# Kernel optimization log

Measured on AMD Instinct MI355X. Metric: run time of the kernel, lower is better.

The kernel has to match this reference:

```python
import jax, jax.numpy as jnp
import numpy as np

B, C, H, W = 2, 256, 64, 64
NUM_HEADS = 8


def setup_inputs() -> dict:
    key = jax.random.key(0)
    k1, k2, k3 = jax.random.split(key, 3)
    x = jax.random.normal(k1, (B, C, H, W), dtype=jnp.float32)
    # 1x1 convs, bias=False -> plain [out_ch, in_ch] matrices
    w_qkv = jax.random.normal(k2, (3 * C, C), dtype=jnp.float32) * (1.0 / np.sqrt(C))
    w_proj = jax.random.normal(k3, (C, C), dtype=jnp.float32) * (1.0 / np.sqrt(C))
    return {"x": x, "w_qkv": w_qkv, "w_proj": w_proj}


def reference(x, w_qkv, w_proj):
    b, c, h, w = x.shape
    hd = NUM_HEADS
    d = c // hd  # head dim
    n = h * w    # number of tokens

    # 1x1 conv == channel matmul: [3C, C] x [B, C, H, W] -> [B, 3C, H, W]
    qkv = jnp.einsum('oc,bchw->bohw', w_qkv, x)
    q, k, v = jnp.split(qkv, 3, axis=1)

    def reshape(t):
        return t.reshape(b, hd, d, n)  # [B, h, d, N]

    q, k, v = map(reshape, (q, k, v))

    # scores[b,h,i,j] = sum_d q[b,h,d,i] * k[b,h,d,j] / sqrt(d)
    scores = jnp.einsum('bhdi,bhdj->bhij', q, k) / jnp.sqrt(jnp.asarray(d, x.dtype))
    attn = jax.nn.softmax(scores, axis=-1)

    # out[b,h,d,i] = sum_j attn[b,h,i,j] * v[b,h,d,j]
    out = jnp.einsum('bhij,bhdj->bhdi', attn, v)
    out = out.reshape(b, c, h, w)

    return jnp.einsum('oc,bchw->bohw', w_proj, out) + x
```

## Files before the change

### kernel.cpp

```cpp
#include <hip/hip_runtime.h>
#include <hip/hip_bf16.h>

#define NB  2
#define CC  256
#define NHD 8
#define HD  32
#define NT  4096

typedef __bf16 bf16x8 __attribute__((ext_vector_type(8)));
typedef bf16x8 bf16x8_ma __attribute__((may_alias));
typedef __bf16 bf16x4 __attribute__((ext_vector_type(4)));
typedef bf16x4 bf16x4_ma __attribute__((may_alias));
typedef float  f32x4  __attribute__((ext_vector_type(4)));
typedef f32x4  f32x4_ma __attribute__((may_alias));
typedef float  f32x16 __attribute__((ext_vector_type(16)));
typedef unsigned int u32x4 __attribute__((ext_vector_type(4)));
typedef unsigned short u16x8 __attribute__((ext_vector_type(8)));

static __device__ __forceinline__ f32x4 zero4() {
    f32x4 z = {0.f, 0.f, 0.f, 0.f}; return z;
}
static __device__ __forceinline__ f32x16 zero16() {
    f32x16 z = {0.f,0.f,0.f,0.f,0.f,0.f,0.f,0.f,
                0.f,0.f,0.f,0.f,0.f,0.f,0.f,0.f};
    return z;
}

#define QSCALE 0.25505392421795654f

#define CVT_PK(dst, lo, hi_) \
    asm("v_cvt_pk_bf16_f32 %0, %1, %2" : "=v"(dst) : "v"(lo), "v"(hi_))
#define PLSWAP(x, y) \
    asm("v_permlane32_swap_b32 %0, %1" : "+v"(x), "+v"(y))


__global__ __launch_bounds__(256) void convw_k(const float* __restrict__ s1,
                                               __bf16* __restrict__ d1, int n1,
                                               const float* __restrict__ s2,
                                               __bf16* __restrict__ d2, int n2) {
    const int i = blockIdx.x * 256 + threadIdx.x;
    if (i < n1) d1[i] = (__bf16)s1[i];
    else if (i - n1 < n2) d2[i - n1] = (__bf16)s2[i - n1];
}

__global__ __launch_bounds__(256) void qkv_k(const __bf16* __restrict__ wqkv,
                                             const float* __restrict__ x,
                                             __bf16* __restrict__ qt,
                                             __bf16* __restrict__ kt,
                                             __bf16* __restrict__ vv) {
    __shared__ __align__(16) __bf16 T[64][264];

    const int tid  = threadIdx.x;
    const int lane = tid & 63, wv = tid >> 6;
    const int g = lane >> 4, c16 = lane & 15;
    const int b    = blockIdx.z;
    const int o0   = blockIdx.y * 64 + wv * 16;
    const int tok0 = blockIdx.x * 64;

    {
        const int tok4 = (tid & 15) * 4;
        const int crow = tid >> 4;
#pragma unroll
        for (int i = 0; i < 16; ++i) {
            const int c = i * 16 + crow;
            f32x4 v = *(const f32x4_ma*)&x[((size_t)(b * CC + c)) * NT + tok0 + tok4];
#pragma unroll
            for (int j = 0; j < 4; ++j)
                T[tok4 + j][c] = (__bf16)v[j];
        }
    }

    const __bf16* arow = wqkv + (size_t)(o0 + c16) * CC + g * 8;
    bf16x8 a[8];
#pragma unroll
    for (int kc = 0; kc < 8; ++kc) a[kc] = *(const bf16x8_ma*)(arow + kc * 32);

    __syncthreads();

    f32x4 acc[4];
#pragma unroll
    for (int i = 0; i < 4; ++i) acc[i] = zero4();

#pragma unroll
    for (int kc = 0; kc < 8; ++kc) {
#pragma unroll
        for (int js = 0; js < 4; ++js) {
            bf16x8 bb = *(const bf16x8_ma*)&T[js * 16 + c16][kc * 32 + g * 8];
            acc[js] = __builtin_amdgcn_mfma_f32_16x16x32_bf16(a[kc], bb, acc[js], 0, 0, 0);
        }
    }

    const int reg = o0 >> 8;
    const int oo0 = (o0 & 255) + g * 4;
    const int h   = oo0 >> 5;
    const int dd0 = oo0 & 31;
    const size_t bh = (size_t)(b * NHD + h);

#pragma unroll
    for (int js = 0; js < 4; ++js) {
        const int tok = tok0 + js * 16 + c16;
        if (reg == 0) {
            bf16x4 pk;
#pragma unroll
            for (int r = 0; r < 4; ++r) pk[r] = (__bf16)(acc[js][r] * QSCALE);
            *(bf16x4_ma*)(qt + (bh * NT + tok) * HD + dd0) = pk;
        } else if (reg == 1) {
            bf16x4 pk;
#pragma unroll
            for (int r = 0; r < 4; ++r) pk[r] = (__bf16)acc[js][r];
            *(bf16x4_ma*)(kt + (bh * NT + tok) * HD + dd0) = pk;
        } else {
#pragma unroll
            for (int r = 0; r < 4; ++r)
                vv[(bh * HD + dd0 + r) * NT + tok] = (__bf16)acc[js][r];
        }
    }
}

__global__ __launch_bounds__(256, 4) void attn_k(const __bf16* __restrict__ qt,
                                                 const __bf16* __restrict__ kt,
                                                 const __bf16* __restrict__ vv,
                                                 __bf16* __restrict__ ao,
                                                 float* __restrict__ PO,
                                                 float* __restrict__ PL) {
    __shared__ __align__(16) __bf16 KF[2][4][2][512];
    __shared__ __align__(16) __bf16 VF[2][4][2][512];

    const int tid  = threadIdx.x;
    const int lane = tid & 63, wv = tid >> 6;
    const int c32 = lane & 31, hi = lane >> 5;
    const int bh = blockIdx.y;
    const int b = bh >> 3, h = bh & 7;
    const int seg = blockIdx.z, nseg = gridDim.z;
    const int i0q = blockIdx.x * 128 + wv * 32;

    const __bf16* qbase = qt + ((size_t)bh * NT + i0q) * HD;
    const __bf16* kbase = kt + (size_t)bh * NT * HD;
    const __bf16* vbase = vv + (size_t)bh * HD * NT;

    bf16x8 aq0 = *(const bf16x8_ma*)(qbase + (size_t)c32 * HD + hi * 8);
    bf16x8 aq1 = *(const bf16x8_ma*)(qbase + (size_t)c32 * HD + 16 + hi * 8);

    u16x8 ones_u = {0x3F80,0x3F80,0x3F80,0x3F80,0x3F80,0x3F80,0x3F80,0x3F80};
    const bf16x8 ones = __builtin_bit_cast(bf16x8, ones_u);

    f32x16 oacc = zero16();
    f32x16 lacc = zero16();

#define STAGE(bf, jb) do {                                                              \
    const __bf16* gk = kbase + (size_t)((jb) + wv * 32 + c32) * HD + hi * 8;            \
    __builtin_amdgcn_global_load_lds(                                                   \
        (const __attribute__((address_space(1))) void*)gk,                              \
        (__attribute__((address_space(3))) void*)&KF[bf][wv][0][0],                     \
        16, 0, 0);                                                                      \
    __builtin_amdgcn_global_load_lds(                                                   \
        (const __attribute__((address_space(1))) void*)(gk + 16),                       \
        (__attribute__((address_space(3))) void*)&KF[bf][wv][1][0],                     \
        16, 0, 0);                                                                      \
    const __bf16* gv = vbase + (size_t)c32 * NT + (jb) + wv * 32 + hi * 8;              \
    __builtin_amdgcn_global_load_lds(                                                   \
        (const __attribute__((address_space(1))) void*)gv,                              \
        (__attribute__((address_space(3))) void*)&VF[bf][wv][0][0],                     \
        16, 0, 0);                                                                      \
    __builtin_amdgcn_global_load_lds(                                                   \
        (const __attribute__((address_space(1))) void*)(gv + 16),                       \
        (__attribute__((address_space(3))) void*)&VF[bf][wv][1][0],                     \
        16, 0, 0);                                                                      \
} while (0)

#define SUBTILE(bf, js) do {                                                            \
    bf16x8 fk0 = *(const bf16x8_ma*)&KF[bf][js][0][lane * 8];                           \
    bf16x8 fk1 = *(const bf16x8_ma*)&KF[bf][js][1][lane * 8];                           \
    bf16x8 fv0 = *(const bf16x8_ma*)&VF[bf][js][0][lane * 8];                           \
    bf16x8 fv1 = *(const bf16x8_ma*)&VF[bf][js][1][lane * 8];                           \
    f32x16 s = __builtin_amdgcn_mfma_f32_32x32x16_bf16(fk0, aq0, zero16(), 0, 0, 0);    \
    s = __builtin_amdgcn_mfma_f32_32x32x16_bf16(fk1, aq1, s, 0, 0, 0);                  \
    float p[16];                                                                        \
    _Pragma("unroll")                                                                   \
    for (int r = 0; r < 16; ++r) p[r] = __builtin_amdgcn_exp2f(s[r]);                   \
    unsigned pk[8];                                                                     \
    _Pragma("unroll")                                                                   \
    for (int i = 0; i < 8; ++i) CVT_PK(pk[i], p[2 * i], p[2 * i + 1]);                  \
    PLSWAP(pk[0], pk[2]);                                                               \
    PLSWAP(pk[1], pk[3]);                                                               \
    PLSWAP(pk[4], pk[6]);                                                               \
    PLSWAP(pk[5], pk[7]);                                                               \
    u32x4 a0 = {pk[0], pk[1], pk[2], pk[3]};                                            \
    u32x4 a1 = {pk[4], pk[5], pk[6], pk[7]};                                            \
    const bf16x8 ap0 = __builtin_bit_cast(bf16x8, a0);                                  \
    const bf16x8 ap1 = __builtin_bit_cast(bf16x8, a1);                                  \
    oacc = __builtin_amdgcn_mfma_f32_32x32x16_bf16(ap0, fv0, oacc, 0, 0, 0);            \
    oacc = __builtin_amdgcn_mfma_f32_32x32x16_bf16(ap1, fv1, oacc, 0, 0, 0);            \
    lacc = __builtin_amdgcn_mfma_f32_32x32x16_bf16(ap0, ones, lacc, 0, 0, 0);           \
    lacc = __builtin_amdgcn_mfma_f32_32x32x16_bf16(ap1, ones, lacc, 0, 0, 0);           \
} while (0)

    const int ntiles  = (NT / 128) / nseg;
    const int j_begin = seg * ntiles * 128;

    STAGE(0, j_begin);
    asm volatile("s_waitcnt vmcnt(0)" ::: "memory");
    __syncthreads();

    int buf = 0;
#pragma unroll 1
    for (int t = 0; t < ntiles; ++t) {
        if (t + 1 < ntiles) STAGE(buf ^ 1, j_begin + (t + 1) * 128);
        SUBTILE(buf, 0);
        SUBTILE(buf, 1);
        SUBTILE(buf, 2);
        SUBTILE(buf, 3);
        asm volatile("s_waitcnt vmcnt(0)" ::: "memory");
        __syncthreads();
        buf ^= 1;
    }

#undef STAGE
#undef SUBTILE

    if (nseg == 1) {
#pragma unroll
        for (int g4 = 0; g4 < 4; ++g4) {
#pragma unroll
            for (int r = 0; r < 4; ++r) {
                const int q = 8 * g4 + 4 * hi + r;
                ao[((size_t)(b * NT) + i0q + q) * CC + h * HD + c32] =
                    (__bf16)(oacc[4 * g4 + r] / lacc[4 * g4 + r]);
            }
        }
    } else {
        float* po = PO + (((size_t)seg * NB * NHD + bh) * NT + i0q) * HD;
#pragma unroll
        for (int g4 = 0; g4 < 4; ++g4) {
#pragma unroll
            for (int r = 0; r < 4; ++r) {
                const int q = 8 * g4 + 4 * hi + r;
                po[(size_t)q * HD + c32] = oacc[4 * g4 + r];
            }
        }
        if (c32 == 0) {
            float* pl = PL + ((size_t)seg * NB * NHD + bh) * NT + i0q;
#pragma unroll
            for (int g4 = 0; g4 < 4; ++g4)
#pragma unroll
                for (int r = 0; r < 4; ++r)
                    pl[8 * g4 + 4 * hi + r] = lacc[4 * g4 + r];
        }
    }
}

__global__ __launch_bounds__(256) void comb_k(const float* __restrict__ PO,
                                              const float* __restrict__ PL,
                                              __bf16* __restrict__ ao,
                                              int nseg) {
    const int i = blockIdx.x * 256 + threadIdx.x;
    const int bh = i >> 15;
    const int rem = i & 32767;
    const int n = rem >> 3, g = rem & 7;
    const int b = bh >> 3, h = bh & 7;

    const size_t SEGO = (size_t)(NB * NHD) * NT * HD;
    const size_t SEGL = (size_t)(NB * NHD) * NT;
    const size_t o0i = (((size_t)bh) * NT + n) * HD + g * 4;
    const size_t li  = (size_t)bh * NT + n;

    f32x4 o = *(const f32x4_ma*)&PO[o0i];
    float l = PL[li];
#pragma unroll 3
    for (int s = 1; s < nseg; ++s) {
        o += *(const f32x4_ma*)&PO[(size_t)s * SEGO + o0i];
        l += PL[(size_t)s * SEGL + li];
    }

    bf16x4 pk;
#pragma unroll
    for (int r = 0; r < 4; ++r) pk[r] = (__bf16)(o[r] / l);
    *(bf16x4_ma*)&ao[((size_t)(b * NT) + n) * CC + h * HD + g * 4] = pk;
}

__global__ __launch_bounds__(256) void proj_k(const __bf16* __restrict__ wp,
                                              const __bf16* __restrict__ ao,
                                              const float* __restrict__ x,
                                              float* __restrict__ out) {
    __shared__ __align__(16) __bf16 BF[4][8][512];

    const int lane = threadIdx.x & 63, wv = threadIdx.x >> 6;
    const int g = lane >> 4, c16 = lane & 15;
    const int b    = blockIdx.z;
    const int o0   = blockIdx.y * 64 + wv * 16;
    const int tok0 = blockIdx.x * 64;

    const __bf16* bsrc = ao + ((size_t)(b * NT + tok0 + wv * 16 + c16)) * CC + g * 8;
#pragma unroll
    for (int kc = 0; kc < 8; ++kc) {
        __builtin_amdgcn_global_load_lds(
            (const __attribute__((address_space(1))) void*)(bsrc + kc * 32),
            (__attribute__((address_space(3))) void*)&BF[wv][kc][0],
            16, 0, 0);
    }

    const __bf16* arow = wp + (size_t)(o0 + c16) * CC + g * 8;
    bf16x8 a[8];
#pragma unroll
    for (int kc = 0; kc < 8; ++kc) a[kc] = *(const bf16x8_ma*)(arow + kc * 32);

    __syncthreads();

    f32x4 acc[4];
#pragma unroll
    for (int i = 0; i < 4; ++i) acc[i] = zero4();

#pragma unroll
    for (int kc = 0; kc < 8; ++kc) {
#pragma unroll
        for (int js = 0; js < 4; ++js) {
            bf16x8 bb = *(const bf16x8_ma*)&BF[js][kc][lane * 8];
            acc[js] = __builtin_amdgcn_mfma_f32_16x16x32_bf16(a[kc], bb, acc[js], 0, 0, 0);
        }
    }

#pragma unroll
    for (int js = 0; js < 4; ++js) {
        const int tok = tok0 + js * 16 + c16;
#pragma unroll
        for (int r = 0; r < 4; ++r) {
            const int o = o0 + g * 4 + r;
            const size_t idx = ((size_t)(b * CC + o)) * NT + tok;
            out[idx] = acc[js][r] + x[idx];
        }
    }
}

extern "C" void kernel_launch(void* const* d_in, const int* in_sizes, int n_in,
                              void* d_out, int out_size, void* d_ws, size_t ws_size,
                              hipStream_t stream) {
    const int SX  = NB * CC * NT;
    const int SW3 = 3 * CC * CC;
    const int SW1 = CC * CC;
    const size_t E = (size_t)SX;

    const float* x  = nullptr;
    const float* wq = nullptr;
    const float* wp = nullptr;
    for (int i = 0; i < n_in; ++i) {
        const int sz = in_sizes[i];
        if (sz == SX || sz == 2 * SX || sz == 4 * SX)           x  = (const float*)d_in[i];
        else if (sz == SW3 || sz == 2 * SW3 || sz == 4 * SW3)   wq = (const float*)d_in[i];
        else if (sz == SW1 || sz == 2 * SW1 || sz == 4 * SW1)   wp = (const float*)d_in[i];
    }
    if (!x || !wq || !wp) {
        x  = (const float*)d_in[0];
        wq = (const float*)d_in[1];
        wp = (const float*)d_in[2];
    }

    __bf16* ws  = (__bf16*)d_ws;
    __bf16* wqb = ws;
    __bf16* wpb = wqb + SW3;
    __bf16* ao  = wpb + SW1;
    __bf16* qt  = ao + E;
    __bf16* kt  = qt + E;
    __bf16* vv  = kt + E;

    const size_t baseB = (size_t)(SW3 + SW1) * 2 + 4 * E * 2;
    const size_t segoB = (size_t)NB * NHD * NT * HD * 4;
    const size_t seglB = (size_t)NB * NHD * NT * 4;
    const int jseg = (ws_size >= baseB + 2 * (segoB + seglB)) ? 2 : 1;
    float* PO = (float*)((char*)d_ws + baseB);
    float* PL = (float*)((char*)d_ws + baseB + (size_t)jseg * segoB);

    float* out = (float*)d_out;

    convw_k<<<dim3((SW3 + SW1 + 255) / 256), 256, 0, stream>>>(wq, wqb, SW3, wp, wpb, SW1);
    qkv_k<<<dim3(NT / 64, (3 * CC) / 64, NB), 256, 0, stream>>>(wqb, x, qt, kt, vv);
    attn_k<<<dim3(NT / 128, NB * NHD, jseg), 256, 0, stream>>>(qt, kt, vv, ao, PO, PL);
    if (jseg > 1)
        comb_k<<<dim3((NB * NHD * NT * (HD / 4)) / 256), 256, 0, stream>>>(PO, PL, ao, jseg);
    proj_k<<<dim3(NT / 64, CC / 64, NB), 256, 0, stream>>>(wpb, ao, x, out);
}
```

Measured before the change: 141.6 us.

## Split K-dimension loads in QKV and proj GEMMs to overlap with MFMA

The QKV and projection kernels now load the first half of the channel dimension, compute MFMAs on it, and only then stage the second half, so global loads overlap with matrix work. The second half of x is held in registers and converted into shared memory after the first compute phase. The attention kernel swaps per-stage address recomputation for incrementing K/V pointers. This adds an extra barrier per block and more register pressure in exchange for hiding load latency.

```diff
diff --git a/kernel.cpp b/kernel.cpp
--- a/kernel.cpp
+++ b/kernel.cpp
@@ -57,17 +57,24 @@
     const int o0   = blockIdx.y * 64 + wv * 16;
     const int tok0 = blockIdx.x * 64;
 
+    const int tok4 = (tid & 15) * 4;
+    const int crow = tid >> 4;
+
     {
-        const int tok4 = (tid & 15) * 4;
-        const int crow = tid >> 4;
-#pragma unroll
-        for (int i = 0; i < 16; ++i) {
+#pragma unroll
+        for (int i = 0; i < 8; ++i) {
             const int c = i * 16 + crow;
             f32x4 v = *(const f32x4_ma*)&x[((size_t)(b * CC + c)) * NT + tok0 + tok4];
 #pragma unroll
-            for (int j = 0; j < 4; ++j)
-                T[tok4 + j][c] = (__bf16)v[j];
-        }
+            for (int j = 0; j < 4; ++j) T[tok4 + j][c] = (__bf16)v[j];
+        }
+    }
+
+    f32x4 v1[8];
+#pragma unroll
+    for (int i = 0; i < 8; ++i) {
+        const int c = 128 + i * 16 + crow;
+        v1[i] = *(const f32x4_ma*)&x[((size_t)(b * CC + c)) * NT + tok0 + tok4];
     }
 
     const __bf16* arow = wqkv + (size_t)(o0 + c16) * CC + g * 8;
@@ -82,7 +89,24 @@
     for (int i = 0; i < 4; ++i) acc[i] = zero4();
 
 #pragma unroll
-    for (int kc = 0; kc < 8; ++kc) {
+    for (int kc = 0; kc < 4; ++kc) {
+#pragma unroll
+        for (int js = 0; js < 4; ++js) {
+            bf16x8 bb = *(const bf16x8_ma*)&T[js * 16 + c16][kc * 32 + g * 8];
+            acc[js] = __builtin_amdgcn_mfma_f32_16x16x32_bf16(a[kc], bb, acc[js], 0, 0, 0);
+        }
+    }
+
+#pragma unroll
+    for (int i = 0; i < 8; ++i) {
+        const int c = 128 + i * 16 + crow;
+#pragma unroll
+        for (int j = 0; j < 4; ++j) T[tok4 + j][c] = (__bf16)v1[i][j];
+    }
+    __syncthreads();
+
+#pragma unroll
+    for (int kc = 4; kc < 8; ++kc) {
 #pragma unroll
         for (int js = 0; js < 4; ++js) {
             bf16x8 bb = *(const bf16x8_ma*)&T[js * 16 + c16][kc * 32 + g * 8];
@@ -147,25 +171,31 @@
     f32x16 oacc = zero16();
     f32x16 lacc = zero16();
 
-#define STAGE(bf, jb) do {                                                              \
-    const __bf16* gk = kbase + (size_t)((jb) + wv * 32 + c32) * HD + hi * 8;            \
+    const int ntiles  = (NT / 128) / nseg;
+    const int j_begin = seg * ntiles * 128;
+
+    const __bf16* kp = kbase + (size_t)(j_begin + wv * 32 + c32) * HD + hi * 8;
+    const __bf16* vp = vbase + (size_t)c32 * NT + j_begin + wv * 32 + hi * 8;
+
+#define STAGE(bf) do {                                                                  \
     __builtin_amdgcn_global_load_lds(                                                   \
-        (const __attribute__((address_space(1))) void*)gk,                              \
+        (const __attribute__((address_space(1))) void*)kp,                              \
         (__attribute__((address_space(3))) void*)&KF[bf][wv][0][0],                     \
         16, 0, 0);                                                                      \
     __builtin_amdgcn_global_load_lds(                                                   \
-        (const __attribute__((address_space(1))) void*)(gk + 16),                       \
+        (const __attribute__((address_space(1))) void*)(kp + 16),                       \
         (__attribute__((address_space(3))) void*)&KF[bf][wv][1][0],                     \
         16, 0, 0);                                                                      \
-    const __bf16* gv = vbase + (size_t)c32 * NT + (jb) + wv * 32 + hi * 8;              \
     __builtin_amdgcn_global_load_lds(                                                   \
-        (const __attribute__((address_space(1))) void*)gv,                              \
+        (const __attribute__((address_space(1))) void*)vp,                              \
         (__attribute__((address_space(3))) void*)&VF[bf][wv][0][0],                     \
         16, 0, 0);                                                                      \
     __builtin_amdgcn_global_load_lds(                                                   \
-        (const __attribute__((address_space(1))) void*)(gv + 16),                       \
+        (const __attribute__((address_space(1))) void*)(vp + 16),                       \
         (__attribute__((address_space(3))) void*)&VF[bf][wv][1][0],                     \
         16, 0, 0);                                                                      \
+    kp += (size_t)128 * HD;                                                             \
+    vp += 128;                                                                          \
 } while (0)
 
 #define SUBTILE(bf, js) do {                                                            \
@@ -195,17 +225,14 @@
     lacc = __builtin_amdgcn_mfma_f32_32x32x16_bf16(ap1, ones, lacc, 0, 0, 0);           \
 } while (0)
 
-    const int ntiles  = (NT / 128) / nseg;
-    const int j_begin = seg * ntiles * 128;
-
-    STAGE(0, j_begin);
+    STAGE(0);
     asm volatile("s_waitcnt vmcnt(0)" ::: "memory");
     __syncthreads();
 
     int buf = 0;
 #pragma unroll 1
     for (int t = 0; t < ntiles; ++t) {
-        if (t + 1 < ntiles) STAGE(buf ^ 1, j_begin + (t + 1) * 128);
+        if (t + 1 < ntiles) STAGE(buf ^ 1);
         SUBTILE(buf, 0);
         SUBTILE(buf, 1);
         SUBTILE(buf, 2);
@@ -292,7 +319,7 @@
 
     const __bf16* bsrc = ao + ((size_t)(b * NT + tok0 + wv * 16 + c16)) * CC + g * 8;
 #pragma unroll
-    for (int kc = 0; kc < 8; ++kc) {
+    for (int kc = 0; kc < 4; ++kc) {
         __builtin_amdgcn_global_load_lds(
             (const __attribute__((address_space(1))) void*)(bsrc + kc * 32),
             (__attribute__((address_space(3))) void*)&BF[wv][kc][0],
@@ -306,12 +333,32 @@
 
     __syncthreads();
 
+#pragma unroll
+    for (int kc = 4; kc < 8; ++kc) {
+        __builtin_amdgcn_global_load_lds(
+            (const __attribute__((address_space(1))) void*)(bsrc + kc * 32),
+            (__attribute__((address_space(3))) void*)&BF[wv][kc][0],
+            16, 0, 0);
+    }
+
     f32x4 acc[4];
 #pragma unroll
     for (int i = 0; i < 4; ++i) acc[i] = zero4();
 
 #pragma unroll
-    for (int kc = 0; kc < 8; ++kc) {
+    for (int kc = 0; kc < 4; ++kc) {
+#pragma unroll
+        for (int js = 0; js < 4; ++js) {
+            bf16x8 bb = *(const bf16x8_ma*)&BF[js][kc][lane * 8];
+            acc[js] = __builtin_amdgcn_mfma_f32_16x16x32_bf16(a[kc], bb, acc[js], 0, 0, 0);
+        }
+    }
+
+    asm volatile("s_waitcnt vmcnt(0)" ::: "memory");
+    __syncthreads();
+
+#pragma unroll
+    for (int kc = 4; kc < 8; ++kc) {
 #pragma unroll
         for (int js = 0; js < 4; ++js) {
             bf16x8 bb = *(const bf16x8_ma*)&BF[js][kc][lane * 8];
```

After: 140.2 us. No clear change (-1.0%).
